# Kernel optimization log

Hardware: AMD Instinct MI355X
Metric: run time of the kernel (lower is better)

Reference implementation:

```python
import jax, jax.numpy as jnp
import numpy as np

BT = 80        # B*T frames (B=8, T=10)
MAX_N = 13     # cfg.num_boxes
K2D = 26400    # K*K*D = 5*5*1056 (crop_size^2 * emb_features)
NFB = 1024     # cfg.num_features_boxes
A = 6          # cfg.num_actions
G = 5          # cfg.num_activities


def setup_inputs() -> dict:
    key = jax.random.key(0)
    k = jax.random.split(key, 8)
    # RoIAlign box features, already flattened per box: [BT, MAX_N, K*K*D]
    boxes_features_flat = jax.random.normal(k[0], (BT, MAX_N, K2D), jnp.float32)
    # ragged per-frame box counts in [1, MAX_N]
    bboxes_num = jax.random.randint(k[1], (BT,), 1, MAX_N + 1, dtype=jnp.int32)
    # kaiming-normal linear weights (fan_in scaling), zero biases (per nn.Linear default bias ~0 scale)
    w_emb = jax.random.normal(k[2], (K2D, NFB), jnp.float32) * np.float32(np.sqrt(2.0 / K2D))
    b_emb = jnp.zeros((NFB,), jnp.float32)
    w_act = jax.random.normal(k[3], (NFB, A), jnp.float32) * np.float32(np.sqrt(2.0 / NFB))
    b_act = jnp.zeros((A,), jnp.float32)
    w_acty = jax.random.normal(k[4], (NFB, G), jnp.float32) * np.float32(np.sqrt(2.0 / NFB))
    b_acty = jnp.zeros((G,), jnp.float32)
    return {
        "boxes_features_flat": boxes_features_flat,
        "w_emb": w_emb, "b_emb": b_emb,
        "w_act": w_act, "b_act": b_act,
        "w_acty": w_acty, "b_acty": b_acty,
        "bboxes_num": bboxes_num,
    }


def reference(boxes_features_flat, w_emb, b_emb, w_act, b_act, w_acty, b_acty, bboxes_num):
    # fc_emb_1 + ReLU (dropout is identity at inference)
    h = jax.nn.relu(jnp.einsum('bnk,kf->bnf', boxes_features_flat, w_emb) + b_emb)  # [BT, MAX_N, NFB]
    # validity mask replacing the per-frame ragged slice boxes_features_all[bt, :N]
    mask = jnp.arange(MAX_N)[None, :] < bboxes_num[:, None]  # [BT, MAX_N]
    # per-box action scores; invalid (padded) boxes zeroed
    actions_scores = (jnp.einsum('bnf,fa->bna', h, w_act) + b_act) * mask[..., None].astype(h.dtype)
    # masked max-pool over valid boxes per frame (N >= 1 always)
    neg = jnp.finfo(h.dtype).min
    pooled = jnp.max(jnp.where(mask[..., None], h, neg), axis=1)  # [BT, NFB]
    activities_scores = pooled @ w_acty + b_acty  # [BT, G]
    return actions_scores, activities_scores
```

## Files before the change

### kernel.cpp

```cpp
#include <hip/hip_runtime.h>

#define K2D 26400
#define NFB 1024
#define NBT 80
#define MAXN 13
#define MTOT (NBT * MAXN)
#define NA 6
#define NG 5
#define KITERS 825
#define TILEB 8192
#define MT128 9
#define MT256 5
#define NT 8

typedef __attribute__((ext_vector_type(8))) short     bf16x8;
typedef __attribute__((ext_vector_type(4))) float     f32x4;
typedef __attribute__((ext_vector_type(4))) unsigned short us4;
typedef __attribute__((ext_vector_type(8))) unsigned short us8;

__device__ __forceinline__ unsigned short f2bf(float x) {
    unsigned u = __float_as_uint(x);
    u += 0x7fffu + ((u >> 16) & 1u);
    return (unsigned short)(u >> 16);
}

__device__ __forceinline__ void gload_lds16(const void* g, void* l) {
    __builtin_amdgcn_global_load_lds(
        (const __attribute__((address_space(1))) unsigned int*)g,
        (__attribute__((address_space(3))) unsigned int*)l, 16, 0, 0);
}

#define META_OFFS 1
#define META_MAP  82

__global__ __launch_bounds__(256) void prefix_kernel(const int* __restrict__ nb,
                                                     int* __restrict__ meta)
{
    __shared__ int off[NBT + 1];
    const int t = threadIdx.x;
    if (t == 0) {
        int acc = 0;
        for (int i = 0; i < NBT; ++i) { off[i] = acc; acc += nb[i]; }
        off[NBT] = acc;
        meta[0] = acc;
    }
    __syncthreads();
    if (t < NBT + 1) meta[META_OFFS + t] = off[t];
    for (int f = t; f < NBT * MAXN; f += 256) {
        const int bt = f / MAXN, n = f % MAXN;
        if (n < off[bt + 1] - off[bt]) meta[META_MAP + off[bt] + n] = f;
    }
}

__global__ __launch_bounds__(256) void pack_a(const float* __restrict__ A,
                                              const int* __restrict__ meta,
                                              unsigned short* __restrict__ out)
{
    const int bm = blockIdx.x, it = blockIdx.y;
    const int total = meta[0];
    if (bm * 128 >= total) return;
    __shared__ __attribute__((aligned(16))) unsigned short T[4][128][8];
    const int t = threadIdx.x, k0 = it * 32;
#pragma unroll
    for (int i = 0; i < 4; ++i) {
        const int f  = t + i * 256;
        const int m  = f >> 3;
        const int kp = (f & 7) * 4;
        const int p  = bm * 128 + m;
        float4 v = {0.f, 0.f, 0.f, 0.f};
        if (p < total) {
            const int src = meta[META_MAP + p];
            v = *(const float4*)(A + (size_t)src * K2D + k0 + kp);
        }
        us4 u = { f2bf(v.x), f2bf(v.y), f2bf(v.z), f2bf(v.w) };
        *(us4*)(&T[kp >> 3][m][kp & 7]) = u;
    }
    __syncthreads();
    us8* o = (us8*)(out + (size_t)(bm * KITERS + it) * (TILEB / 2));
    const us8* s = (const us8*)&T[0][0][0];
#pragma unroll
    for (int i = 0; i < 2; ++i) { const int c = t + i * 256; o[c] = s[c]; }
}

__global__ __launch_bounds__(256) void pack_b(const float* __restrict__ B,
                                              unsigned short* __restrict__ out)
{
    __shared__ float S[32][129];
    const int bn = blockIdx.x, it = blockIdx.y;
    const int t = threadIdx.x;
#pragma unroll
    for (int i = 0; i < 4; ++i) {
        const int f  = t + i * 256;
        const int kr = f >> 5;
        const int n4 = (f & 31) * 4;
        const float4 v = *(const float4*)(B + (size_t)(it * 32 + kr) * NFB + bn * 128 + n4);
        S[kr][n4 + 0] = v.x; S[kr][n4 + 1] = v.y;
        S[kr][n4 + 2] = v.z; S[kr][n4 + 3] = v.w;
    }
    __syncthreads();
    unsigned short* o = out + (size_t)(bn * KITERS + it) * (TILEB / 2);
#pragma unroll
    for (int i = 0; i < 2; ++i) {
        const int c = t + i * 256;
        const int n = c & 127, q = c >> 7;
        us8 u;
#pragma unroll
        for (int j = 0; j < 8; ++j) u[j] = f2bf(S[q * 8 + j][n]);
        *(us8*)(o + c * 8) = u;
    }
}

__global__ __launch_bounds__(512, 2) void gemm_pipe(
    const unsigned short* __restrict__ Apack,
    const unsigned short* __restrict__ Bpack,
    float* __restrict__ Cp,
    const int* __restrict__ meta, int kchunk)
{
    __shared__ __attribute__((aligned(16))) unsigned short buf[3][3][4][128][8];
    const int bm = blockIdx.x, bn = blockIdx.y, s = blockIdx.z;
    const int total = meta[0];
    if (bm * 256 >= total) return;

    const int t = threadIdx.x;
    const int wave = t >> 6, lane = t & 63;
    const int quad = lane >> 4, l16 = lane & 15;
    const int wmq = wave & 3;
    const int asel = wmq >> 1;
    const int wm128 = (wmq & 1) * 64;
    const int wn = (wave >> 2) * 64;
    const int it0 = s * kchunk;
    const int it1 = min(KITERS, it0 + kchunk);

    f32x4 acc[4][4] = {};

    if (it0 < it1) {
        const int itlast = it1 - 1;
        const char* A0 = (const char*)Apack + (size_t)(2 * bm) * KITERS * TILEB;
        const char* A1 = (const char*)Apack + (size_t)(2 * bm + 1) * KITERS * TILEB;
        const char* Bb = (const char*)Bpack + (size_t)bn * KITERS * TILEB;
        const int go = t * 16;
        const int lo = wave * 1024;

#define ISSUE(IT, ST) do {                                                     \
    const size_t o_ = (size_t)(IT) * TILEB;                                    \
    gload_lds16(A0 + o_ + go, (char*)&buf[ST][0] + lo);                        \
    gload_lds16(A1 + o_ + go, (char*)&buf[ST][1] + lo);                        \
    gload_lds16(Bb + o_ + go, (char*)&buf[ST][2] + lo);                        \
} while (0)

        ISSUE(it0, 0);
        { const int itp = min(it0 + 1, itlast); ISSUE(itp, 1); }

#define STEP(ITV, CUR, DST) do {                                               \
    asm volatile("" ::: "memory");                                             \
    __builtin_amdgcn_s_waitcnt(0x1F73);                          \
    __builtin_amdgcn_s_barrier();                                              \
    asm volatile("" ::: "memory");                                             \
    int itn = (ITV) + 2; itn = itn > itlast ? itlast : itn;                    \
    ISSUE(itn, DST);                                                           \
    bf16x8 af[4], bfr[4];                                                      \
    _Pragma("unroll")                                                          \
    for (int x = 0; x < 4; ++x) {                                              \
        af[x]  = *(const bf16x8*)(&buf[CUR][asel][quad][wm128 + x * 16 + l16][0]); \
        bfr[x] = *(const bf16x8*)(&buf[CUR][2][quad][wn + x * 16 + l16][0]);   \
    }                                                                          \
    _Pragma("unroll")                                                          \
    for (int x = 0; x < 4; ++x)                                                \
        _Pragma("unroll")                                                      \
        for (int y = 0; y < 4; ++y)                                            \
            acc[x][y] = __builtin_amdgcn_mfma_f32_16x16x32_bf16(               \
                af[x], bfr[y], acc[x][y], 0, 0, 0);                            \
} while (0)

        for (int it = it0; it < it1; it += 3) {
            STEP(it,     0, 2);
            STEP(it + 1, 1, 0);
            STEP(it + 2, 2, 1);
        }
#undef STEP
#undef ISSUE
    }

#pragma unroll
    for (int x = 0; x < 4; ++x) {
        const int rowb = bm * 256 + wmq * 64 + x * 16 + quad * 4;
#pragma unroll
        for (int y = 0; y < 4; ++y) {
            const int col = bn * 128 + wn + y * 16 + l16;
#pragma unroll
            for (int r = 0; r < 4; ++r) {
                const int rr = rowb + r;
                if (rr < MTOT)
                    Cp[((size_t)s * MTOT + rr) * NFB + col] = acc[x][y][r];
            }
        }
    }
}

__global__ __launch_bounds__(256) void reduce_kernel(
    const float* __restrict__ Cp, const float* __restrict__ b_emb,
    float* __restrict__ h, const int* __restrict__ meta, int splitk)
{
    const int row = blockIdx.x;
    if (row >= meta[0]) return;
    const int t = threadIdx.x;
    const size_t base = (size_t)row * NFB + t * 4;
    float4 v = *(const float4*)(Cp + base);
#pragma unroll 4
    for (int s2 = 1; s2 < splitk; ++s2) {
        const float4 w = *(const float4*)(Cp + (size_t)s2 * MTOT * NFB + base);
        v.x += w.x; v.y += w.y; v.z += w.z; v.w += w.w;
    }
    const float4 be = *(const float4*)(b_emb + t * 4);
    v.x = fmaxf(v.x + be.x, 0.f);
    v.y = fmaxf(v.y + be.y, 0.f);
    v.z = fmaxf(v.z + be.z, 0.f);
    v.w = fmaxf(v.w + be.w, 0.f);
    *(float4*)(h + base) = v;
}

__global__ __launch_bounds__(256) void heads_kernel(
    const float* __restrict__ h,
    const float* __restrict__ w_act,  const float* __restrict__ b_act,
    const float* __restrict__ w_acty, const float* __restrict__ b_acty,
    const int* __restrict__ meta, float* __restrict__ out)
{
    __shared__ __attribute__((aligned(16))) float hs[MAXN][NFB];
    __shared__ float pooled[NFB];
    const int bt = blockIdx.x;
    const int t  = threadIdx.x;
    const int off0 = meta[META_OFFS + bt];
    const int Nb   = meta[META_OFFS + bt + 1] - off0;

    for (int i = 0; i < MAXN; ++i)
        if (i < Nb)
            *(float4*)(&hs[i][t * 4]) =
                *(const float4*)(h + (size_t)(off0 + i) * NFB + t * 4);
    __syncthreads();

    const int wave = t >> 6, lane = t & 63;

    for (int d = wave; d < MAXN * NA; d += 4) {
        const int n = d / NA, a = d % NA;
        if (n < Nb) {
            float sum = 0.f;
            for (int f = lane; f < NFB; f += 64)
                sum += hs[n][f] * w_act[f * NA + a];
#pragma unroll
            for (int o = 32; o > 0; o >>= 1) sum += __shfl_xor(sum, o);
            if (lane == 0) out[bt * (MAXN * NA) + d] = sum + b_act[a];
        } else {
            if (lane == 0) out[bt * (MAXN * NA) + d] = 0.f;
        }
    }

    for (int f = t; f < NFB; f += 256) {
        float m = hs[0][f];
        for (int n2 = 1; n2 < Nb; ++n2) m = fmaxf(m, hs[n2][f]);
        pooled[f] = m;
    }
    __syncthreads();

    for (int g = wave; g < NG; g += 4) {
        float sum = 0.f;
        for (int f = lane; f < NFB; f += 64)
            sum += pooled[f] * w_acty[f * NG + g];
#pragma unroll
        for (int o = 32; o > 0; o >>= 1) sum += __shfl_xor(sum, o);
        if (lane == 0)
            out[NBT * MAXN * NA + bt * NG + g] = sum + b_acty[g];
    }
}

__global__ __launch_bounds__(256) void gemm_f32(
    const float* __restrict__ A, const float* __restrict__ B,
    float* __restrict__ Cp, int kchunk)
{
    __shared__ __attribute__((aligned(16))) unsigned short Alds[4][128][8];
    __shared__ __attribute__((aligned(16))) unsigned short Blds[4][128][8];
    const int t = threadIdx.x;
    const int bm = blockIdx.x, bn = blockIdx.y, s = blockIdx.z;
    const int wave = t >> 6, lane = t & 63;
    const int quad = lane >> 4, l16 = lane & 15;
    const int wm = (wave & 1) * 64, wn = (wave >> 1) * 64;
    const int row0 = bm * 128, col0 = bn * 128;
    const int it0 = s * kchunk, it1 = min(KITERS, it0 + kchunk);

    f32x4 acc[4][4] = {};
    for (int it = it0; it < it1; ++it) {
        const int k0 = it * 32;
#pragma unroll
        for (int i = 0; i < 4; ++i) {
            const int f = t + i * 256, m = f >> 3, kp = (f & 7) * 4;
            const int gr = row0 + m;
            float4 v = {0.f, 0.f, 0.f, 0.f};
            if (gr < MTOT) v = *(const float4*)(A + (size_t)gr * K2D + k0 + kp);
            us4 u = { f2bf(v.x), f2bf(v.y), f2bf(v.z), f2bf(v.w) };
            *(us4*)(&Alds[kp >> 3][m][kp & 7]) = u;
        }
#pragma unroll
        for (int i = 0; i < 2; ++i) {
            const int p = t + i * 256, n = p & 127, kq = p >> 7;
            const float* bp = B + (size_t)(k0 + kq * 8) * NFB + (col0 + n);
            us8 u;
#pragma unroll
            for (int j = 0; j < 8; ++j) u[j] = f2bf(bp[(size_t)j * NFB]);
            *(us8*)(&Blds[kq][n][0]) = u;
        }
        __syncthreads();
        bf16x8 af[4], bfr[4];
#pragma unroll
        for (int x = 0; x < 4; ++x) {
            af[x]  = *(const bf16x8*)(&Alds[quad][wm + x * 16 + l16][0]);
            bfr[x] = *(const bf16x8*)(&Blds[quad][wn + x * 16 + l16][0]);
        }
#pragma unroll
        for (int x = 0; x < 4; ++x)
#pragma unroll
            for (int y = 0; y < 4; ++y)
                acc[x][y] = __builtin_amdgcn_mfma_f32_16x16x32_bf16(
                    af[x], bfr[y], acc[x][y], 0, 0, 0);
        __syncthreads();
    }
#pragma unroll
    for (int x = 0; x < 4; ++x) {
        const int rowb = row0 + wm + x * 16 + quad * 4;
#pragma unroll
        for (int y = 0; y < 4; ++y) {
            const int col = col0 + wn + y * 16 + l16;
#pragma unroll
            for (int r = 0; r < 4; ++r) {
                const int rr = rowb + r;
                if (rr < MTOT)
                    Cp[((size_t)s * MTOT + rr) * NFB + col] = acc[x][y][r];
            }
        }
    }
}

__global__ __launch_bounds__(256) void finalize_fallback(
    const float* __restrict__ Cp, const float* __restrict__ b_emb,
    const float* __restrict__ w_act, const float* __restrict__ b_act,
    const float* __restrict__ w_acty, const float* __restrict__ b_acty,
    const int* __restrict__ bboxes_num, float* __restrict__ out, int splitk)
{
    __shared__ __attribute__((aligned(16))) float h[MAXN][NFB];
    __shared__ float pooled[NFB];
    const int bt = blockIdx.x;
    const int t  = threadIdx.x;
    const int Nb = bboxes_num[bt];

    for (int i = 0; i < MAXN; ++i) {
        const int flat = i * 256 + t;
        const int row  = flat >> 8;
        const int f4   = flat & 255;
        const size_t base = ((size_t)(bt * MAXN + row)) * NFB + f4 * 4;
        float4 v = *(const float4*)(Cp + base);
        for (int s2 = 1; s2 < splitk; ++s2) {
            const float4 w = *(const float4*)(Cp + (size_t)s2 * MTOT * NFB + base);
            v.x += w.x; v.y += w.y; v.z += w.z; v.w += w.w;
        }
        const float4 be = *(const float4*)(b_emb + f4 * 4);
        v.x = fmaxf(v.x + be.x, 0.f);
        v.y = fmaxf(v.y + be.y, 0.f);
        v.z = fmaxf(v.z + be.z, 0.f);
        v.w = fmaxf(v.w + be.w, 0.f);
        *(float4*)(&h[row][f4 * 4]) = v;
    }
    __syncthreads();
    const int wave = t >> 6, lane = t & 63;
    for (int d = wave; d < MAXN * NA; d += 4) {
        const int n = d / NA, a = d % NA;
        float sum = 0.f;
        for (int f = lane; f < NFB; f += 64)
            sum += h[n][f] * w_act[f * NA + a];
#pragma unroll
        for (int o = 32; o > 0; o >>= 1) sum += __shfl_xor(sum, o);
        if (lane == 0)
            out[bt * (MAXN * NA) + d] = (n < Nb) ? (sum + b_act[a]) : 0.f;
    }
    for (int f = t; f < NFB; f += 256) {
        float m = h[0][f];
        for (int n2 = 1; n2 < Nb; ++n2) m = fmaxf(m, h[n2][f]);
        pooled[f] = m;
    }
    __syncthreads();
    for (int g = wave; g < NG; g += 4) {
        float sum = 0.f;
        for (int f = lane; f < NFB; f += 64)
            sum += pooled[f] * w_acty[f * NG + g];
#pragma unroll
        for (int o = 32; o > 0; o >>= 1) sum += __shfl_xor(sum, o);
        if (lane == 0)
            out[NBT * MAXN * NA + bt * NG + g] = sum + b_acty[g];
    }
}

extern "C" void kernel_launch(void* const* d_in, const int* in_sizes, int n_in,
                              void* d_out, int out_size, void* d_ws, size_t ws_size,
                              hipStream_t stream) {
    const float* A      = (const float*)d_in[0];
    const float* W      = (const float*)d_in[1];
    const float* b_emb  = (const float*)d_in[2];
    const float* w_act  = (const float*)d_in[3];
    const float* b_act  = (const float*)d_in[4];
    const float* w_acty = (const float*)d_in[5];
    const float* b_acty = (const float*)d_in[6];
    const int*   bboxes = (const int*)d_in[7];
    float* out = (float*)d_out;

    const size_t PACKA = (size_t)MT128 * KITERS * TILEB;
    const size_t PACKB = (size_t)NT * KITERS * TILEB;
    const size_t PART  = (size_t)MTOT * NFB * 4;
    const size_t METAB = 8192;

    if (ws_size >= PACKA + PACKB + 5 * PART + METAB) {
        int splitk = (int)((ws_size - PACKA - PACKB - PART - METAB) / PART);
        if (splitk > 16) splitk = 16;
        const int kchunk = ((KITERS + 3 * splitk - 1) / (3 * splitk)) * 3;

        unsigned short* Ap = (unsigned short*)d_ws;
        unsigned short* Bp = (unsigned short*)((char*)d_ws + PACKA);
        float* Cp = (float*)((char*)d_ws + PACKA + PACKB);
        float* h  = (float*)((char*)d_ws + PACKA + PACKB + (size_t)splitk * PART);
        int* meta = (int*)((char*)d_ws + PACKA + PACKB + (size_t)(splitk + 1) * PART);

        prefix_kernel<<<1, 256, 0, stream>>>(bboxes, meta);
        pack_a<<<dim3(MT128, KITERS), 256, 0, stream>>>(A, meta, Ap);
        pack_b<<<dim3(NT, KITERS), 256, 0, stream>>>(W, Bp);
        gemm_pipe<<<dim3(MT256, NT, splitk), 512, 0, stream>>>(Ap, Bp, Cp, meta, kchunk);
        reduce_kernel<<<MTOT, 256, 0, stream>>>(Cp, b_emb, h, meta, splitk);
        heads_kernel<<<NBT, 256, 0, stream>>>(h, w_act, b_act, w_acty, b_acty,
                                              meta, out);
    } else {
        float* Cp = (float*)d_ws;
        gemm_f32<<<dim3(MT128, NT, 4), 256, 0, stream>>>(A, W, Cp, 207);
        finalize_fallback<<<NBT, 256, 0, stream>>>(Cp, b_emb, w_act, b_act,
                                                   w_acty, b_acty, bboxes, out, 4);
    }
}
```

Measured before the change: 374.2 us.

## Widen GEMM tile to 256x256, reorder grid, raise split-K, parallelize prefix scan

The bf16 GEMM block tile grows from 256x128 to 256x256, so each wave holds 4x8 MFMA accumulators and each LDS stage loads two B tiles, raising the arithmetic per byte staged. The grid is reordered so N-tiles vary fastest, and split-K can now go up to 20 chunks, with the real chunk count passed to the reduce. Packing A now uses 10 M-tiles, pack_b reads global memory directly without an LDS transpose, and the prefix sum becomes a parallel Hillis-Steele scan. Costs are higher register pressure from 128 accumulator floats per thread at 2 waves/SIMD, more LDS per block, and h now reusing the start of the workspace where the packed A lives.

New measurement: 354.8 us. 5.2% less time.

```diff
diff --git a/kernel.cpp b/kernel.cpp
--- a/kernel.cpp
+++ b/kernel.cpp
@@ -9,9 +9,10 @@
 #define NG 5
 #define KITERS 825
 #define TILEB 8192
-#define MT128 9
+#define AIMG 10
+#define NT128 8
 #define MT256 5
-#define NT 8
+#define NT256 4
 
 typedef __attribute__((ext_vector_type(8))) short     bf16x8;
 typedef __attribute__((ext_vector_type(4))) float     f32x4;
@@ -36,19 +37,24 @@
 __global__ __launch_bounds__(256) void prefix_kernel(const int* __restrict__ nb,
                                                      int* __restrict__ meta)
 {
-    __shared__ int off[NBT + 1];
+    __shared__ int a[128];
     const int t = threadIdx.x;
-    if (t == 0) {
-        int acc = 0;
-        for (int i = 0; i < NBT; ++i) { off[i] = acc; acc += nb[i]; }
-        off[NBT] = acc;
-        meta[0] = acc;
-    }
-    __syncthreads();
-    if (t < NBT + 1) meta[META_OFFS + t] = off[t];
+    if (t < 128) a[t] = (t < NBT) ? nb[t] : 0;
+    __syncthreads();
+#pragma unroll
+    for (int s = 1; s < 128; s <<= 1) {
+        int v = 0;
+        if (t < 128 && t >= s) v = a[t - s];
+        __syncthreads();
+        if (t < 128) a[t] += v;
+        __syncthreads();
+    }
+    if (t == 0) { meta[0] = a[NBT - 1]; meta[META_OFFS] = 0; }
+    if (t < NBT) meta[META_OFFS + t + 1] = a[t];
     for (int f = t; f < NBT * MAXN; f += 256) {
         const int bt = f / MAXN, n = f % MAXN;
-        if (n < off[bt + 1] - off[bt]) meta[META_MAP + off[bt] + n] = f;
+        const int o0 = bt ? a[bt - 1] : 0;
+        if (n < a[bt] - o0) meta[META_MAP + o0 + n] = f;
     }
 }
 
@@ -85,27 +91,20 @@
 __global__ __launch_bounds__(256) void pack_b(const float* __restrict__ B,
                                               unsigned short* __restrict__ out)
 {
-    __shared__ float S[32][129];
     const int bn = blockIdx.x, it = blockIdx.y;
     const int t = threadIdx.x;
-#pragma unroll
-    for (int i = 0; i < 4; ++i) {
-        const int f  = t + i * 256;
-        const int kr = f >> 5;
-        const int n4 = (f & 31) * 4;
-        const float4 v = *(const float4*)(B + (size_t)(it * 32 + kr) * NFB + bn * 128 + n4);
-        S[kr][n4 + 0] = v.x; S[kr][n4 + 1] = v.y;
-        S[kr][n4 + 2] = v.z; S[kr][n4 + 3] = v.w;
-    }
-    __syncthreads();
     unsigned short* o = out + (size_t)(bn * KITERS + it) * (TILEB / 2);
 #pragma unroll
     for (int i = 0; i < 2; ++i) {
         const int c = t + i * 256;
         const int n = c & 127, q = c >> 7;
+        const float* bp = B + (size_t)(it * 32 + q * 8) * NFB + bn * 128 + n;
+        float v[8];
+#pragma unroll
+        for (int j = 0; j < 8; ++j) v[j] = bp[(size_t)j * NFB];
         us8 u;
 #pragma unroll
-        for (int j = 0; j < 8; ++j) u[j] = f2bf(S[q * 8 + j][n]);
+        for (int j = 0; j < 8; ++j) u[j] = f2bf(v[j]);
         *(us8*)(o + c * 8) = u;
     }
 }
@@ -116,8 +115,8 @@
     float* __restrict__ Cp,
     const int* __restrict__ meta, int kchunk)
 {
-    __shared__ __attribute__((aligned(16))) unsigned short buf[3][3][4][128][8];
-    const int bm = blockIdx.x, bn = blockIdx.y, s = blockIdx.z;
+    __shared__ __attribute__((aligned(16))) unsigned short buf[3][4][4][128][8];
+    const int bn = blockIdx.x, s = blockIdx.y, bm = blockIdx.z;
     const int total = meta[0];
     if (bm * 256 >= total) return;
 
@@ -127,17 +126,18 @@
     const int wmq = wave & 3;
     const int asel = wmq >> 1;
     const int wm128 = (wmq & 1) * 64;
-    const int wn = (wave >> 2) * 64;
+    const int bsel = wave >> 2;
     const int it0 = s * kchunk;
     const int it1 = min(KITERS, it0 + kchunk);
 
-    f32x4 acc[4][4] = {};
-
-    if (it0 < it1) {
+    f32x4 acc[4][8] = {};
+
+    {
         const int itlast = it1 - 1;
         const char* A0 = (const char*)Apack + (size_t)(2 * bm) * KITERS * TILEB;
         const char* A1 = (const char*)Apack + (size_t)(2 * bm + 1) * KITERS * TILEB;
-        const char* Bb = (const char*)Bpack + (size_t)bn * KITERS * TILEB;
+        const char* B0 = (const char*)Bpack + (size_t)(2 * bn) * KITERS * TILEB;
+        const char* B1 = (const char*)Bpack + (size_t)(2 * bn + 1) * KITERS * TILEB;
         const int go = t * 16;
         const int lo = wave * 1024;
 
@@ -145,7 +145,8 @@
     const size_t o_ = (size_t)(IT) * TILEB;                                    \
     gload_lds16(A0 + o_ + go, (char*)&buf[ST][0] + lo);                        \
     gload_lds16(A1 + o_ + go, (char*)&buf[ST][1] + lo);                        \
-    gload_lds16(Bb + o_ + go, (char*)&buf[ST][2] + lo);                        \
+    gload_lds16(B0 + o_ + go, (char*)&buf[ST][2] + lo);                        \
+    gload_lds16(B1 + o_ + go, (char*)&buf[ST][3] + lo);                        \
 } while (0)
 
         ISSUE(it0, 0);
@@ -153,21 +154,22 @@
 
 #define STEP(ITV, CUR, DST) do {                                               \
     asm volatile("" ::: "memory");                                             \
-    __builtin_amdgcn_s_waitcnt(0x1F73);                          \
+    __builtin_amdgcn_s_waitcnt(0xF74);                           \
     __builtin_amdgcn_s_barrier();                                              \
     asm volatile("" ::: "memory");                                             \
     int itn = (ITV) + 2; itn = itn > itlast ? itlast : itn;                    \
     ISSUE(itn, DST);                                                           \
-    bf16x8 af[4], bfr[4];                                                      \
+    bf16x8 af[4], bfr[8];                                                      \
     _Pragma("unroll")                                                          \
-    for (int x = 0; x < 4; ++x) {                                              \
-        af[x]  = *(const bf16x8*)(&buf[CUR][asel][quad][wm128 + x * 16 + l16][0]); \
-        bfr[x] = *(const bf16x8*)(&buf[CUR][2][quad][wn + x * 16 + l16][0]);   \
-    }                                                                          \
+    for (int x = 0; x < 4; ++x)                                                \
+        af[x] = *(const bf16x8*)(&buf[CUR][asel][quad][wm128 + x * 16 + l16][0]); \
+    _Pragma("unroll")                                                          \
+    for (int y = 0; y < 8; ++y)                                                \
+        bfr[y] = *(const bf16x8*)(&buf[CUR][2 + bsel][quad][y * 16 + l16][0]); \
     _Pragma("unroll")                                                          \
     for (int x = 0; x < 4; ++x)                                                \
         _Pragma("unroll")                                                      \
-        for (int y = 0; y < 4; ++y)                                            \
+        for (int y = 0; y < 8; ++y)                                            \
             acc[x][y] = __builtin_amdgcn_mfma_f32_16x16x32_bf16(               \
                 af[x], bfr[y], acc[x][y], 0, 0, 0);                            \
 } while (0)
@@ -185,8 +187,8 @@
     for (int x = 0; x < 4; ++x) {
         const int rowb = bm * 256 + wmq * 64 + x * 16 + quad * 4;
 #pragma unroll
-        for (int y = 0; y < 4; ++y) {
-            const int col = bn * 128 + wn + y * 16 + l16;
+        for (int y = 0; y < 8; ++y) {
+            const int col = bn * 256 + bsel * 128 + y * 16 + l16;
 #pragma unroll
             for (int r = 0; r < 4; ++r) {
                 const int rr = rowb + r;
@@ -409,32 +411,36 @@
     const int*   bboxes = (const int*)d_in[7];
     float* out = (float*)d_out;
 
-    const size_t PACKA = (size_t)MT128 * KITERS * TILEB;
-    const size_t PACKB = (size_t)NT * KITERS * TILEB;
+    const size_t PACKA = (size_t)AIMG * KITERS * TILEB;
+    const size_t PACKB = (size_t)NT128 * KITERS * TILEB;
     const size_t PART  = (size_t)MTOT * NFB * 4;
     const size_t METAB = 8192;
 
-    if (ws_size >= PACKA + PACKB + 5 * PART + METAB) {
-        int splitk = (int)((ws_size - PACKA - PACKB - PART - METAB) / PART);
-        if (splitk > 16) splitk = 16;
+    long avail = (long)ws_size - (long)(PACKA + PACKB + METAB);
+    int splitk = (int)(avail / (long)PART);
+    if (splitk > 20) splitk = 20;
+
+    if (splitk >= 4) {
         const int kchunk = ((KITERS + 3 * splitk - 1) / (3 * splitk)) * 3;
+        const int nchunks = (KITERS + kchunk - 1) / kchunk;
 
         unsigned short* Ap = (unsigned short*)d_ws;
         unsigned short* Bp = (unsigned short*)((char*)d_ws + PACKA);
         float* Cp = (float*)((char*)d_ws + PACKA + PACKB);
-        float* h  = (float*)((char*)d_ws + PACKA + PACKB + (size_t)splitk * PART);
-        int* meta = (int*)((char*)d_ws + PACKA + PACKB + (size_t)(splitk + 1) * PART);
+        int* meta = (int*)((char*)d_ws + PACKA + PACKB + (size_t)splitk * PART);
+        float* h  = (float*)d_ws;
 
         prefix_kernel<<<1, 256, 0, stream>>>(bboxes, meta);
-        pack_a<<<dim3(MT128, KITERS), 256, 0, stream>>>(A, meta, Ap);
-        pack_b<<<dim3(NT, KITERS), 256, 0, stream>>>(W, Bp);
-        gemm_pipe<<<dim3(MT256, NT, splitk), 512, 0, stream>>>(Ap, Bp, Cp, meta, kchunk);
-        reduce_kernel<<<MTOT, 256, 0, stream>>>(Cp, b_emb, h, meta, splitk);
+        pack_a<<<dim3(AIMG, KITERS), 256, 0, stream>>>(A, meta, Ap);
+        pack_b<<<dim3(NT128, KITERS), 256, 0, stream>>>(W, Bp);
+        gemm_pipe<<<dim3(NT256, nchunks, MT256), 512, 0, stream>>>(Ap, Bp, Cp,
+                                                                   meta, kchunk);
+        reduce_kernel<<<MTOT, 256, 0, stream>>>(Cp, b_emb, h, meta, nchunks);
         heads_kernel<<<NBT, 256, 0, stream>>>(h, w_act, b_act, w_acty, b_acty,
                                               meta, out);
     } else {
         float* Cp = (float*)d_ws;
-        gemm_f32<<<dim3(MT128, NT, 4), 256, 0, stream>>>(A, W, Cp, 207);
+        gemm_f32<<<dim3(9, 8, 4), 256, 0, stream>>>(A, W, Cp, 207);
         finalize_fallback<<<NBT, 256, 0, stream>>>(Cp, b_emb, w_act, b_act,
                                                    w_acty, b_acty, bboxes, out, 4);
     }
```
